# Kernel tuning notes

Hardware: AMD Instinct MI355X
Metric: run time of the kernel (lower is better)

Reference implementation:

```python
import jax, jax.numpy as jnp
import numpy as np


def setup_inputs() -> dict:
    key = jax.random.key(0)
    ks = jax.random.split(key, 8)
    B, C, W, H = 4, 256, 64, 64
    dqk = C // 8
    s_in = 1.0 / np.sqrt(C)
    return {
        "x": jax.random.normal(ks[0], (B, C, W, H), dtype=jnp.float32),
        "Wq": jax.random.normal(ks[1], (dqk, C), dtype=jnp.float32) * s_in,
        "bq": jnp.zeros((dqk,), dtype=jnp.float32),
        "Wk": jax.random.normal(ks[2], (dqk, C), dtype=jnp.float32) * s_in,
        "bk": jnp.zeros((dqk,), dtype=jnp.float32),
        "Wv": jax.random.normal(ks[3], (C, C), dtype=jnp.float32) * s_in,
        "bv": jnp.zeros((C,), dtype=jnp.float32),
        "gamma": jnp.zeros((1,), dtype=jnp.float32),
    }


def reference(x, Wq, bq, Wk, bk, Wv, bv, gamma):
    B, C, W, H = x.shape
    N = W * H
    xf = x.reshape(B, C, N)  # flatten spatial: B x C x N
    # 1x1 convs == per-pixel linear projections over channels
    q = jnp.einsum("bcn,dc->bnd", xf, Wq) + bq            # B x N x dqk
    k = jnp.einsum("bcn,dc->bdn", xf, Wk) + bk[None, :, None]  # B x dqk x N
    v = jnp.einsum("bcn,dc->bdn", xf, Wv) + bv[None, :, None]  # B x C x N
    # unscaled attention, softmax over keys (last dim)
    attn = jax.nn.softmax(jnp.einsum("bnd,bdm->bnm", q, k), axis=-1)  # B x N x N
    # out[b,c,i] = sum_j v[b,c,j] * attn[b,i,j]  (bmm with attn^T)
    out = jnp.einsum("bcj,bij->bci", v, attn).reshape(B, C, W, H)
    return gamma[0] * out + x
```

## Files before the change

kernel.cpp:

```cpp
#include <hip/hip_runtime.h>

#define BB 4
#define CC 256
#define NN 4096

typedef __attribute__((ext_vector_type(8))) short bh8;
typedef __attribute__((ext_vector_type(4))) float f32x4;

#define WPK_OFF  0
#define BALL_OFF 163840
#define QBF_OFF  165888
#define KBF_OFF  (165888 + 1048576)
#define VBF_OFF  (165888 + 2097152)

typedef const __attribute__((address_space(1))) void* gas_t;
typedef __attribute__((address_space(3))) void* las_t;
__device__ inline void gld16(const void* g, void* l) {
    __builtin_amdgcn_global_load_lds((gas_t)g, (las_t)l, 16, 0, 0);
}

__device__ inline int pack2bf(float a, float b) {
    unsigned ua = __builtin_bit_cast(unsigned, a) + 0x8000u;
    unsigned ub = __builtin_bit_cast(unsigned, b) + 0x8000u;
    return (int)__builtin_amdgcn_perm(ub, ua, 0x07060302u);
}
__device__ inline short f2bf1(float a) {
    return (short)((__builtin_bit_cast(unsigned, a) + 0x8000u) >> 16);
}

__global__ __launch_bounds__(256) void prep_w(const float* __restrict__ Wq,
        const float* __restrict__ bq, const float* __restrict__ Wk,
        const float* __restrict__ bk, const float* __restrict__ Wv,
        const float* __restrict__ bv, short* __restrict__ Wpk,
        float* __restrict__ ball) {
    int tid = blockIdx.x * 256 + threadIdx.x;
    if (tid < 10240) {
        int lane = tid & 63;
        int fc = tid >> 6;
        int mt = fc >> 3, ck = fc & 7;
        int m = mt * 16 + (lane & 15);
        int c0 = ck * 32 + (lane >> 4) * 8;
        const float* wrow;
        if (m < 32)      wrow = Wq + m * 256;
        else if (m < 64) wrow = Wk + (m - 32) * 256;
        else             wrow = Wv + (m - 64) * 256;
        int d[4];
        #pragma unroll
        for (int p = 0; p < 4; ++p)
            d[p] = pack2bf(wrow[c0 + 2 * p], wrow[c0 + 2 * p + 1]);
        *(int4*)(Wpk + tid * 8) = make_int4(d[0], d[1], d[2], d[3]);
    }
    if (tid < 320) {
        float b2 = tid < 32 ? bq[tid] : (tid < 64 ? bk[tid - 32] : bv[tid - 64]);
        ball[tid] = b2;
    }
}

__global__ __launch_bounds__(256) void proj(const float* __restrict__ x,
        const short* __restrict__ Wpk, const float* __restrict__ ball,
        short* __restrict__ qbf, short* __restrict__ kbf,
        short* __restrict__ vbf) {
    int t = threadIdx.x;
    int w = t >> 6, lane = t & 63, quad = lane >> 4, c15 = lane & 15;
    int tile = blockIdx.x;
    int b = tile >> 8, n0 = (tile & 255) * 16;
    const float* xb = x + (size_t)b * CC * NN;

    bh8 af[8];
    #pragma unroll
    for (int ck = 0; ck < 8; ++ck) {
        float v[8];
        #pragma unroll
        for (int e = 0; e < 8; ++e)
            v[e] = xb[(size_t)(ck * 32 + quad * 8 + e) * NN + n0 + c15];
        int d[4];
        #pragma unroll
        for (int p = 0; p < 4; ++p) d[p] = pack2bf(v[2 * p], v[2 * p + 1]);
        af[ck] = __builtin_bit_cast(bh8, make_int4(d[0], d[1], d[2], d[3]));
    }

    #pragma unroll
    for (int mti = 0; mti < 5; ++mti) {
        int mt = w * 5 + mti;
        float bl = ball[mt * 16 + c15];
        f32x4 acc = {bl, bl, bl, bl};
        #pragma unroll
        for (int ck = 0; ck < 8; ++ck) {
            bh8 wf = *(const bh8*)(Wpk + ((mt * 8 + ck) * 64 + lane) * 8);
            acc = __builtin_amdgcn_mfma_f32_16x16x32_bf16(af[ck], wf, acc, 0, 0, 0);
        }
        if (mt < 4) {
            short* dst = (mt < 2) ? qbf : kbf;
            int m = (mt & 1) * 16 + c15;
            #pragma unroll
            for (int r = 0; r < 4; ++r)
                dst[(size_t)(b * NN + n0 + quad * 4 + r) * 32 + m] = f2bf1(acc[r]);
        } else {
            int c = mt * 16 + c15 - 64;
            int2 pk;
            pk.x = pack2bf(acc[0], acc[1]);
            pk.y = pack2bf(acc[2], acc[3]);
            *(int2*)(vbf + (size_t)b * CC * NN + (size_t)c * NN + n0 + quad * 4) = pk;
        }
    }
}

__global__ __launch_bounds__(512, 2) void flash_attn(
        const short* __restrict__ qbf, const short* __restrict__ kbf,
        const short* __restrict__ vbf, const float* __restrict__ x,
        const float* __restrict__ gamma, float* __restrict__ out) {
    __shared__ char lds[81920];

    int bid = blockIdx.x;
    int b = bid & 3, i0 = (bid >> 2) * 64;
    int t = threadIdx.x;
    int w = t >> 6, lane = t & 63, quad = lane >> 4, c15 = lane & 15;
    int mg = w & 3, nh = w >> 2, jsub = w & 3;

    const short* qb = qbf + (size_t)b * NN * 32;
    const short* kb = kbf + (size_t)b * NN * 32;
    const short* vb = vbf + (size_t)b * CC * NN;

    bh8 qf0 = *(const bh8*)(qb + (size_t)(i0 + nh * 32 + c15) * 32 + quad * 8);
    bh8 qf1 = *(const bh8*)(qb + (size_t)(i0 + nh * 32 + 16 + c15) * 32 + quad * 8);

    int vrow = w * 32 + (lane >> 3);
    int glog = (lane & 7) ^ ((lane >> 3) & 7);
    const short* vsg = vb + (size_t)vrow * NN + glog * 8;
    char* vdst = lds + w * 4096;

    const short* kptr = kb + (size_t)(jsub * 16 + c15) * 32 + quad * 8;

    char* Pt = lds + 65536;
    float* lred = (float*)lds;

    f32x4 acc[4][2];
    #pragma unroll
    for (int ms = 0; ms < 4; ++ms) {
        acc[ms][0] = (f32x4){0.f, 0.f, 0.f, 0.f};
        acc[ms][1] = (f32x4){0.f, 0.f, 0.f, 0.f};
    }
    float lsum0 = 0.f, lsum1 = 0.f;
    const f32x4 initc = {-12.f, -12.f, -12.f, -12.f};

    #pragma unroll
    for (int r = 0; r < 4; ++r) gld16(vsg + r * 8 * NN, vdst + r * 1024);
    bh8 kf = *(const bh8*)kptr;
    __syncthreads();

    for (int jt = 0; jt < 64; ++jt) {
        int cur = jt & 1;
        f32x4 sa0 = __builtin_amdgcn_mfma_f32_16x16x32_bf16(kf, qf0, initc, 0, 0, 0);
        f32x4 sa1 = __builtin_amdgcn_mfma_f32_16x16x32_bf16(kf, qf1, initc, 0, 0, 0);
        bh8 kfn = *(const bh8*)(kptr + (size_t)((jt + 1) & 63) * 2048);
        float p0[4], p1[4];
        #pragma unroll
        for (int r = 0; r < 4; ++r) {
            p0[r] = __expf(sa0[r]); lsum0 += p0[r];
            p1[r] = __expf(sa1[r]); lsum1 += p1[r];
        }
        char* Ptc = Pt + cur * 8192;
        int g = jsub * 2 + (quad >> 1);
        int pb0 = (nh * 32 + c15) * 128 + ((g ^ (c15 & 7)) * 16) + (quad & 1) * 8;
        *(int2*)(Ptc + pb0) = make_int2(pack2bf(p0[0], p0[1]), pack2bf(p0[2], p0[3]));
        *(int2*)(Ptc + pb0 + 2048) = make_int2(pack2bf(p1[0], p1[1]), pack2bf(p1[2], p1[3]));

        __syncthreads();

        if (jt < 63) {
            const short* vs = vsg + (jt + 1) * 64;
            char* vd = vdst + ((cur ^ 1) << 15);
            #pragma unroll
            for (int r = 0; r < 4; ++r) gld16(vs + r * 8 * NN, vd + r * 1024);
        }

        const char* Vb = lds + cur * 32768;
        #pragma unroll
        for (int kk = 0; kk < 2; ++kk) {
            int gs = ((kk * 4 + quad) ^ (c15 & 7)) * 16;
            bh8 pfa = *(const bh8*)(Ptc + (nh * 32 + c15) * 128 + gs);
            bh8 pfb = *(const bh8*)(Ptc + (nh * 32 + 16 + c15) * 128 + gs);
            #pragma unroll
            for (int ms = 0; ms < 4; ++ms) {
                int c = mg * 64 + ms * 16 + c15;
                bh8 vf = *(const bh8*)(Vb + c * 128 + gs);
                acc[ms][0] = __builtin_amdgcn_mfma_f32_16x16x32_bf16(vf, pfa, acc[ms][0], 0, 0, 0);
                acc[ms][1] = __builtin_amdgcn_mfma_f32_16x16x32_bf16(vf, pfb, acc[ms][1], 0, 0, 0);
            }
        }
        kf = kfn;
    }

    lsum0 += __shfl_xor(lsum0, 16); lsum0 += __shfl_xor(lsum0, 32);
    lsum1 += __shfl_xor(lsum1, 16); lsum1 += __shfl_xor(lsum1, 32);
    __syncthreads();
    if (lane < 16) {
        lred[w * 32 + lane] = lsum0;
        lred[w * 32 + 16 + lane] = lsum1;
    }
    __syncthreads();
    float l0 = lred[(nh * 4 + 0) * 32 + c15] + lred[(nh * 4 + 1) * 32 + c15]
             + lred[(nh * 4 + 2) * 32 + c15] + lred[(nh * 4 + 3) * 32 + c15];
    float l1 = lred[(nh * 4 + 0) * 32 + 16 + c15] + lred[(nh * 4 + 1) * 32 + 16 + c15]
             + lred[(nh * 4 + 2) * 32 + 16 + c15] + lred[(nh * 4 + 3) * 32 + 16 + c15];
    float linv0 = 1.0f / l0, linv1 = 1.0f / l1;

    float gm = gamma[0];
    const float* xb2 = x + (size_t)b * CC * NN;
    float* ob = out + (size_t)b * CC * NN;
    int ia = i0 + nh * 32 + c15, ib2 = ia + 16;
    #pragma unroll
    for (int ms = 0; ms < 4; ++ms) {
        #pragma unroll
        for (int r = 0; r < 4; ++r) {
            int c = mg * 64 + ms * 16 + quad * 4 + r;
            ob[(size_t)c * NN + ia]  = gm * acc[ms][0][r] * linv0 + xb2[(size_t)c * NN + ia];
            ob[(size_t)c * NN + ib2] = gm * acc[ms][1][r] * linv1 + xb2[(size_t)c * NN + ib2];
        }
    }
}

extern "C" void kernel_launch(void* const* d_in, const int* in_sizes, int n_in,
                              void* d_out, int out_size, void* d_ws, size_t ws_size,
                              hipStream_t stream) {
    const float* x     = (const float*)d_in[0];
    const float* Wq    = (const float*)d_in[1];
    const float* bq    = (const float*)d_in[2];
    const float* Wk    = (const float*)d_in[3];
    const float* bk    = (const float*)d_in[4];
    const float* Wv    = (const float*)d_in[5];
    const float* bv    = (const float*)d_in[6];
    const float* gamma = (const float*)d_in[7];
    float* out = (float*)d_out;
    char*  ws  = (char*)d_ws;
    short* Wpk  = (short*)(ws + WPK_OFF);
    float* ball = (float*)(ws + BALL_OFF);
    short* qbf  = (short*)(ws + QBF_OFF);
    short* kbf  = (short*)(ws + KBF_OFF);
    short* vbf  = (short*)(ws + VBF_OFF);

    prep_w<<<40, 256, 0, stream>>>(Wq, bq, Wk, bk, Wv, bv, Wpk, ball);
    proj<<<1024, 256, 0, stream>>>(x, Wpk, ball, qbf, kbf, vbf);
    flash_attn<<<256, 512, 0, stream>>>(qbf, kbf, vbf, x, gamma, out);
}
```

Baseline: 146.3 us.

## Load V fragments directly from global into registers, drop V LDS staging

```diff
diff --git a/kernel.cpp b/kernel.cpp
--- a/kernel.cpp
+++ b/kernel.cpp
@@ -109,13 +109,13 @@
         const short* __restrict__ qbf, const short* __restrict__ kbf,
         const short* __restrict__ vbf, const float* __restrict__ x,
         const float* __restrict__ gamma, float* __restrict__ out) {
-    __shared__ char lds[81920];
+    __shared__ char lds[17408];
 
     int bid = blockIdx.x;
     int b = bid & 3, i0 = (bid >> 2) * 64;
     int t = threadIdx.x;
     int w = t >> 6, lane = t & 63, quad = lane >> 4, c15 = lane & 15;
-    int mg = w & 3, nh = w >> 2, jsub = w & 3;
+    int nh = w >> 2, jsub = w & 3;
 
     const short* qb = qbf + (size_t)b * NN * 32;
     const short* kb = kbf + (size_t)b * NN * 32;
@@ -124,35 +124,36 @@
     bh8 qf0 = *(const bh8*)(qb + (size_t)(i0 + nh * 32 + c15) * 32 + quad * 8);
     bh8 qf1 = *(const bh8*)(qb + (size_t)(i0 + nh * 32 + 16 + c15) * 32 + quad * 8);
 
-    int vrow = w * 32 + (lane >> 3);
-    int glog = (lane & 7) ^ ((lane >> 3) & 7);
-    const short* vsg = vb + (size_t)vrow * NN + glog * 8;
-    char* vdst = lds + w * 4096;
-
     const short* kptr = kb + (size_t)(jsub * 16 + c15) * 32 + quad * 8;
 
-    char* Pt = lds + 65536;
-    float* lred = (float*)lds;
-
-    f32x4 acc[4][2];
-    #pragma unroll
-    for (int ms = 0; ms < 4; ++ms) {
-        acc[ms][0] = (f32x4){0.f, 0.f, 0.f, 0.f};
-        acc[ms][1] = (f32x4){0.f, 0.f, 0.f, 0.f};
-    }
+    const short* vp0 = vb + (size_t)(w * 32 + c15) * NN + quad * 8;
+    const short* vp1 = vp0 + (size_t)16 * NN;
+
+    char* Pt = lds;
+    float* lred = (float*)(lds + 16384);
+
+    f32x4 acc[2][4];
+    #pragma unroll
+    for (int ms = 0; ms < 2; ++ms)
+        #pragma unroll
+        for (int f = 0; f < 4; ++f) acc[ms][f] = (f32x4){0.f, 0.f, 0.f, 0.f};
+
     float lsum0 = 0.f, lsum1 = 0.f;
     const f32x4 initc = {-12.f, -12.f, -12.f, -12.f};
 
-    #pragma unroll
-    for (int r = 0; r < 4; ++r) gld16(vsg + r * 8 * NN, vdst + r * 1024);
     bh8 kf = *(const bh8*)kptr;
-    __syncthreads();
 
     for (int jt = 0; jt < 64; ++jt) {
         int cur = jt & 1;
+        bh8 kfn = *(const bh8*)(kptr + (size_t)((jt + 1) & 63) * 2048);
+        size_t jo = (size_t)jt * 64;
+        bh8 vf00 = *(const bh8*)(vp0 + jo);
+        bh8 vf01 = *(const bh8*)(vp1 + jo);
+        bh8 vf10 = *(const bh8*)(vp0 + jo + 32);
+        bh8 vf11 = *(const bh8*)(vp1 + jo + 32);
+
         f32x4 sa0 = __builtin_amdgcn_mfma_f32_16x16x32_bf16(kf, qf0, initc, 0, 0, 0);
         f32x4 sa1 = __builtin_amdgcn_mfma_f32_16x16x32_bf16(kf, qf1, initc, 0, 0, 0);
-        bh8 kfn = *(const bh8*)(kptr + (size_t)((jt + 1) & 63) * 2048);
         float p0[4], p1[4];
         #pragma unroll
         for (int r = 0; r < 4; ++r) {
@@ -167,55 +168,54 @@
 
         __syncthreads();
 
-        if (jt < 63) {
-            const short* vs = vsg + (jt + 1) * 64;
-            char* vd = vdst + ((cur ^ 1) << 15);
-            #pragma unroll
-            for (int r = 0; r < 4; ++r) gld16(vs + r * 8 * NN, vd + r * 1024);
-        }
-
-        const char* Vb = lds + cur * 32768;
         #pragma unroll
         for (int kk = 0; kk < 2; ++kk) {
             int gs = ((kk * 4 + quad) ^ (c15 & 7)) * 16;
-            bh8 pfa = *(const bh8*)(Ptc + (nh * 32 + c15) * 128 + gs);
-            bh8 pfb = *(const bh8*)(Ptc + (nh * 32 + 16 + c15) * 128 + gs);
-            #pragma unroll
-            for (int ms = 0; ms < 4; ++ms) {
-                int c = mg * 64 + ms * 16 + c15;
-                bh8 vf = *(const bh8*)(Vb + c * 128 + gs);
-                acc[ms][0] = __builtin_amdgcn_mfma_f32_16x16x32_bf16(vf, pfa, acc[ms][0], 0, 0, 0);
-                acc[ms][1] = __builtin_amdgcn_mfma_f32_16x16x32_bf16(vf, pfb, acc[ms][1], 0, 0, 0);
-            }
+            bh8 pf[4];
+            #pragma unroll
+            for (int f = 0; f < 4; ++f)
+                pf[f] = *(const bh8*)(Ptc + (f * 16 + c15) * 128 + gs);
+            bh8 va = kk ? vf10 : vf00;
+            bh8 vbb = kk ? vf11 : vf01;
+            #pragma unroll
+            for (int f = 0; f < 4; ++f)
+                acc[0][f] = __builtin_amdgcn_mfma_f32_16x16x32_bf16(va, pf[f], acc[0][f], 0, 0, 0);
+            #pragma unroll
+            for (int f = 0; f < 4; ++f)
+                acc[1][f] = __builtin_amdgcn_mfma_f32_16x16x32_bf16(vbb, pf[f], acc[1][f], 0, 0, 0);
         }
         kf = kfn;
     }
 
     lsum0 += __shfl_xor(lsum0, 16); lsum0 += __shfl_xor(lsum0, 32);
     lsum1 += __shfl_xor(lsum1, 16); lsum1 += __shfl_xor(lsum1, 32);
-    __syncthreads();
     if (lane < 16) {
         lred[w * 32 + lane] = lsum0;
         lred[w * 32 + 16 + lane] = lsum1;
     }
     __syncthreads();
-    float l0 = lred[(nh * 4 + 0) * 32 + c15] + lred[(nh * 4 + 1) * 32 + c15]
-             + lred[(nh * 4 + 2) * 32 + c15] + lred[(nh * 4 + 3) * 32 + c15];
-    float l1 = lred[(nh * 4 + 0) * 32 + 16 + c15] + lred[(nh * 4 + 1) * 32 + 16 + c15]
-             + lred[(nh * 4 + 2) * 32 + 16 + c15] + lred[(nh * 4 + 3) * 32 + 16 + c15];
-    float linv0 = 1.0f / l0, linv1 = 1.0f / l1;
+    float linv[4];
+    #pragma unroll
+    for (int f = 0; f < 4; ++f) {
+        int base = (f >> 1) * 4 * 32 + (f & 1) * 16 + c15;
+        linv[f] = 1.0f / (lred[base] + lred[base + 32]
+                        + lred[base + 64] + lred[base + 96]);
+    }
 
     float gm = gamma[0];
     const float* xb2 = x + (size_t)b * CC * NN;
     float* ob = out + (size_t)b * CC * NN;
-    int ia = i0 + nh * 32 + c15, ib2 = ia + 16;
-    #pragma unroll
-    for (int ms = 0; ms < 4; ++ms) {
-        #pragma unroll
-        for (int r = 0; r < 4; ++r) {
-            int c = mg * 64 + ms * 16 + quad * 4 + r;
-            ob[(size_t)c * NN + ia]  = gm * acc[ms][0][r] * linv0 + xb2[(size_t)c * NN + ia];
-            ob[(size_t)c * NN + ib2] = gm * acc[ms][1][r] * linv1 + xb2[(size_t)c * NN + ib2];
+    #pragma unroll
+    for (int ms = 0; ms < 2; ++ms) {
+        #pragma unroll
+        for (int f = 0; f < 4; ++f) {
+            int i = i0 + f * 16 + c15;
+            #pragma unroll
+            for (int r = 0; r < 4; ++r) {
+                int c = w * 32 + ms * 16 + quad * 4 + r;
+                ob[(size_t)c * NN + i] = gm * acc[ms][f][r] * linv[f]
+                                       + xb2[(size_t)c * NN + i];
+            }
         }
     }
 }
```

Result: slower. 163.6 us (+11.8%).

## Process two key tiles per barrier with four-deep V and P LDS buffering

Applied to the files above, without the earlier changes.

```diff
diff --git a/kernel.cpp b/kernel.cpp
--- a/kernel.cpp
+++ b/kernel.cpp
@@ -109,7 +109,7 @@
         const short* __restrict__ qbf, const short* __restrict__ kbf,
         const short* __restrict__ vbf, const float* __restrict__ x,
         const float* __restrict__ gamma, float* __restrict__ out) {
-    __shared__ char lds[81920];
+    __shared__ char lds[163840];
 
     int bid = blockIdx.x;
     int b = bid & 3, i0 = (bid >> 2) * 64;
@@ -127,11 +127,10 @@
     int vrow = w * 32 + (lane >> 3);
     int glog = (lane & 7) ^ ((lane >> 3) & 7);
     const short* vsg = vb + (size_t)vrow * NN + glog * 8;
-    char* vdst = lds + w * 4096;
 
     const short* kptr = kb + (size_t)(jsub * 16 + c15) * 32 + quad * 8;
 
-    char* Pt = lds + 65536;
+    char* Pt = lds + 131072;
     float* lred = (float*)lds;
 
     f32x4 acc[4][2];
@@ -144,51 +143,73 @@
     const f32x4 initc = {-12.f, -12.f, -12.f, -12.f};
 
     #pragma unroll
-    for (int r = 0; r < 4; ++r) gld16(vsg + r * 8 * NN, vdst + r * 1024);
-    bh8 kf = *(const bh8*)kptr;
+    for (int r = 0; r < 4; ++r) gld16(vsg + r * 8 * NN, lds + w * 4096 + r * 1024);
+    #pragma unroll
+    for (int r = 0; r < 4; ++r) gld16(vsg + 64 + r * 8 * NN, lds + 32768 + w * 4096 + r * 1024);
+    bh8 kfa = *(const bh8*)kptr;
+    bh8 kfb = *(const bh8*)(kptr + 2048);
     __syncthreads();
 
-    for (int jt = 0; jt < 64; ++jt) {
-        int cur = jt & 1;
-        f32x4 sa0 = __builtin_amdgcn_mfma_f32_16x16x32_bf16(kf, qf0, initc, 0, 0, 0);
-        f32x4 sa1 = __builtin_amdgcn_mfma_f32_16x16x32_bf16(kf, qf1, initc, 0, 0, 0);
-        bh8 kfn = *(const bh8*)(kptr + (size_t)((jt + 1) & 63) * 2048);
-        float p0[4], p1[4];
+    int g = jsub * 2 + (quad >> 1);
+    int pb0 = (nh * 32 + c15) * 128 + ((g ^ (c15 & 7)) * 16) + (quad & 1) * 8;
+
+    for (int pr = 0; pr < 32; ++pr) {
+        int jt0 = pr * 2, jt1 = jt0 + 1;
+        int ba = jt0 & 3, bb = jt1 & 3;
+        f32x4 sa0a = __builtin_amdgcn_mfma_f32_16x16x32_bf16(kfa, qf0, initc, 0, 0, 0);
+        f32x4 sa1a = __builtin_amdgcn_mfma_f32_16x16x32_bf16(kfa, qf1, initc, 0, 0, 0);
+        f32x4 sa0b = __builtin_amdgcn_mfma_f32_16x16x32_bf16(kfb, qf0, initc, 0, 0, 0);
+        f32x4 sa1b = __builtin_amdgcn_mfma_f32_16x16x32_bf16(kfb, qf1, initc, 0, 0, 0);
+        bh8 kfan = *(const bh8*)(kptr + (size_t)((jt0 + 2) & 63) * 2048);
+        bh8 kfbn = *(const bh8*)(kptr + (size_t)((jt1 + 2) & 63) * 2048);
+        float pa0[4], pa1[4], pb0v[4], pb1v[4];
         #pragma unroll
         for (int r = 0; r < 4; ++r) {
-            p0[r] = __expf(sa0[r]); lsum0 += p0[r];
-            p1[r] = __expf(sa1[r]); lsum1 += p1[r];
-        }
-        char* Ptc = Pt + cur * 8192;
-        int g = jsub * 2 + (quad >> 1);
-        int pb0 = (nh * 32 + c15) * 128 + ((g ^ (c15 & 7)) * 16) + (quad & 1) * 8;
-        *(int2*)(Ptc + pb0) = make_int2(pack2bf(p0[0], p0[1]), pack2bf(p0[2], p0[3]));
-        *(int2*)(Ptc + pb0 + 2048) = make_int2(pack2bf(p1[0], p1[1]), pack2bf(p1[2], p1[3]));
+            pa0[r] = __expf(sa0a[r]); lsum0 += pa0[r];
+            pa1[r] = __expf(sa1a[r]); lsum1 += pa1[r];
+            pb0v[r] = __expf(sa0b[r]); lsum0 += pb0v[r];
+            pb1v[r] = __expf(sa1b[r]); lsum1 += pb1v[r];
+        }
+        char* Pa = Pt + ba * 8192;
+        char* Pb = Pt + bb * 8192;
+        *(int2*)(Pa + pb0) = make_int2(pack2bf(pa0[0], pa0[1]), pack2bf(pa0[2], pa0[3]));
+        *(int2*)(Pa + pb0 + 2048) = make_int2(pack2bf(pa1[0], pa1[1]), pack2bf(pa1[2], pa1[3]));
+        *(int2*)(Pb + pb0) = make_int2(pack2bf(pb0v[0], pb0v[1]), pack2bf(pb0v[2], pb0v[3]));
+        *(int2*)(Pb + pb0 + 2048) = make_int2(pack2bf(pb1v[0], pb1v[1]), pack2bf(pb1v[2], pb1v[3]));
 
         __syncthreads();
 
-        if (jt < 63) {
-            const short* vs = vsg + (jt + 1) * 64;
-            char* vd = vdst + ((cur ^ 1) << 15);
-            #pragma unroll
-            for (int r = 0; r < 4; ++r) gld16(vs + r * 8 * NN, vd + r * 1024);
-        }
-
-        const char* Vb = lds + cur * 32768;
-        #pragma unroll
-        for (int kk = 0; kk < 2; ++kk) {
-            int gs = ((kk * 4 + quad) ^ (c15 & 7)) * 16;
-            bh8 pfa = *(const bh8*)(Ptc + (nh * 32 + c15) * 128 + gs);
-            bh8 pfb = *(const bh8*)(Ptc + (nh * 32 + 16 + c15) * 128 + gs);
-            #pragma unroll
-            for (int ms = 0; ms < 4; ++ms) {
-                int c = mg * 64 + ms * 16 + c15;
-                bh8 vf = *(const bh8*)(Vb + c * 128 + gs);
-                acc[ms][0] = __builtin_amdgcn_mfma_f32_16x16x32_bf16(vf, pfa, acc[ms][0], 0, 0, 0);
-                acc[ms][1] = __builtin_amdgcn_mfma_f32_16x16x32_bf16(vf, pfb, acc[ms][1], 0, 0, 0);
+        {
+            const short* vsA = vsg + (size_t)((jt0 + 2) & 63) * 64;
+            const short* vsB = vsg + (size_t)((jt1 + 2) & 63) * 64;
+            char* vdA = lds + (size_t)(ba ^ 2) * 32768 + w * 4096;
+            char* vdB = lds + (size_t)(bb ^ 2) * 32768 + w * 4096;
+            #pragma unroll
+            for (int r = 0; r < 4; ++r) gld16(vsA + r * 8 * NN, vdA + r * 1024);
+            #pragma unroll
+            for (int r = 0; r < 4; ++r) gld16(vsB + r * 8 * NN, vdB + r * 1024);
+        }
+
+        #pragma unroll
+        for (int st = 0; st < 2; ++st) {
+            const char* Vb = lds + (size_t)(st ? bb : ba) * 32768;
+            const char* Ptc = st ? Pb : Pa;
+            #pragma unroll
+            for (int kk = 0; kk < 2; ++kk) {
+                int gs = ((kk * 4 + quad) ^ (c15 & 7)) * 16;
+                bh8 pfa = *(const bh8*)(Ptc + (nh * 32 + c15) * 128 + gs);
+                bh8 pfb = *(const bh8*)(Ptc + (nh * 32 + 16 + c15) * 128 + gs);
+                #pragma unroll
+                for (int ms = 0; ms < 4; ++ms) {
+                    int c = mg * 64 + ms * 16 + c15;
+                    bh8 vf = *(const bh8*)(Vb + c * 128 + gs);
+                    acc[ms][0] = __builtin_amdgcn_mfma_f32_16x16x32_bf16(vf, pfa, acc[ms][0], 0, 0, 0);
+                    acc[ms][1] = __builtin_amdgcn_mfma_f32_16x16x32_bf16(vf, pfb, acc[ms][1], 0, 0, 0);
+                }
             }
         }
-        kf = kfn;
+        kfa = kfan;
+        kfb = kfbn;
     }
 
     lsum0 += __shfl_xor(lsum0, 16); lsum0 += __shfl_xor(lsum0, 32);
```

After: 144.6 us. Within noise of the previous version (-1.2%).

## Keep P in registers and split keys across waves with LDS reduction

Applied to the files above, without the earlier changes.

```diff
diff --git a/kernel.cpp b/kernel.cpp
--- a/kernel.cpp
+++ b/kernel.cpp
@@ -5,6 +5,7 @@
 #define NN 4096
 
 typedef __attribute__((ext_vector_type(8))) short bh8;
+typedef __attribute__((ext_vector_type(4))) short bh4;
 typedef __attribute__((ext_vector_type(4))) float f32x4;
 
 #define WPK_OFF  0
@@ -109,36 +110,35 @@
         const short* __restrict__ qbf, const short* __restrict__ kbf,
         const short* __restrict__ vbf, const float* __restrict__ x,
         const float* __restrict__ gamma, float* __restrict__ out) {
-    __shared__ char lds[81920];
+    __shared__ char lds[136192];
 
     int bid = blockIdx.x;
     int b = bid & 3, i0 = (bid >> 2) * 64;
     int t = threadIdx.x;
     int w = t >> 6, lane = t & 63, quad = lane >> 4, c15 = lane & 15;
-    int mg = w & 3, nh = w >> 2, jsub = w & 3;
+    int jsub = w & 3, ih = w >> 2;
 
     const short* qb = qbf + (size_t)b * NN * 32;
     const short* kb = kbf + (size_t)b * NN * 32;
     const short* vb = vbf + (size_t)b * CC * NN;
 
-    bh8 qf0 = *(const bh8*)(qb + (size_t)(i0 + nh * 32 + c15) * 32 + quad * 8);
-    bh8 qf1 = *(const bh8*)(qb + (size_t)(i0 + nh * 32 + 16 + c15) * 32 + quad * 8);
-
-    int vrow = w * 32 + (lane >> 3);
+    bh8 qf0 = *(const bh8*)(qb + (size_t)(i0 + ih * 32 + c15) * 32 + quad * 8);
+    bh8 qf1 = *(const bh8*)(qb + (size_t)(i0 + ih * 32 + 16 + c15) * 32 + quad * 8);
+
     int glog = (lane & 7) ^ ((lane >> 3) & 7);
-    const short* vsg = vb + (size_t)vrow * NN + glog * 8;
+    const short* vsg = vb + (size_t)(w * 32 + (lane >> 3)) * NN + glog * 8;
     char* vdst = lds + w * 4096;
 
     const short* kptr = kb + (size_t)(jsub * 16 + c15) * 32 + quad * 8;
 
-    char* Pt = lds + 65536;
-    float* lred = (float*)lds;
-
-    f32x4 acc[4][2];
-    #pragma unroll
-    for (int ms = 0; ms < 4; ++ms) {
-        acc[ms][0] = (f32x4){0.f, 0.f, 0.f, 0.f};
-        acc[ms][1] = (f32x4){0.f, 0.f, 0.f, 0.f};
+    int gb = jsub * 2 + (quad >> 1);
+    int vrd = c15 * 128 + ((gb ^ (c15 & 7)) << 4) + (quad & 1) * 8;
+
+    f32x4 acc[16][2];
+    #pragma unroll
+    for (int cb = 0; cb < 16; ++cb) {
+        acc[cb][0] = (f32x4){0.f, 0.f, 0.f, 0.f};
+        acc[cb][1] = (f32x4){0.f, 0.f, 0.f, 0.f};
     }
     float lsum0 = 0.f, lsum1 = 0.f;
     const f32x4 initc = {-12.f, -12.f, -12.f, -12.f};
@@ -159,11 +159,10 @@
             p0[r] = __expf(sa0[r]); lsum0 += p0[r];
             p1[r] = __expf(sa1[r]); lsum1 += p1[r];
         }
-        char* Ptc = Pt + cur * 8192;
-        int g = jsub * 2 + (quad >> 1);
-        int pb0 = (nh * 32 + c15) * 128 + ((g ^ (c15 & 7)) * 16) + (quad & 1) * 8;
-        *(int2*)(Ptc + pb0) = make_int2(pack2bf(p0[0], p0[1]), pack2bf(p0[2], p0[3]));
-        *(int2*)(Ptc + pb0 + 2048) = make_int2(pack2bf(p1[0], p1[1]), pack2bf(p1[2], p1[3]));
+        int2 a2 = make_int2(pack2bf(p0[0], p0[1]), pack2bf(p0[2], p0[3]));
+        int2 b2 = make_int2(pack2bf(p1[0], p1[1]), pack2bf(p1[2], p1[3]));
+        bh4 pA = __builtin_bit_cast(bh4, a2);
+        bh4 pB = __builtin_bit_cast(bh4, b2);
 
         __syncthreads();
 
@@ -176,47 +175,66 @@
 
         const char* Vb = lds + cur * 32768;
         #pragma unroll
-        for (int kk = 0; kk < 2; ++kk) {
-            int gs = ((kk * 4 + quad) ^ (c15 & 7)) * 16;
-            bh8 pfa = *(const bh8*)(Ptc + (nh * 32 + c15) * 128 + gs);
-            bh8 pfb = *(const bh8*)(Ptc + (nh * 32 + 16 + c15) * 128 + gs);
-            #pragma unroll
-            for (int ms = 0; ms < 4; ++ms) {
-                int c = mg * 64 + ms * 16 + c15;
-                bh8 vf = *(const bh8*)(Vb + c * 128 + gs);
-                acc[ms][0] = __builtin_amdgcn_mfma_f32_16x16x32_bf16(vf, pfa, acc[ms][0], 0, 0, 0);
-                acc[ms][1] = __builtin_amdgcn_mfma_f32_16x16x32_bf16(vf, pfb, acc[ms][1], 0, 0, 0);
-            }
+        for (int cb = 0; cb < 16; ++cb) {
+            bh4 vf = *(const bh4*)(Vb + cb * 2048 + vrd);
+            acc[cb][0] = __builtin_amdgcn_mfma_f32_16x16x16bf16_1k(vf, pA, acc[cb][0], 0, 0, 0);
+            acc[cb][1] = __builtin_amdgcn_mfma_f32_16x16x16bf16_1k(vf, pB, acc[cb][1], 0, 0, 0);
         }
         kf = kfn;
     }
 
     lsum0 += __shfl_xor(lsum0, 16); lsum0 += __shfl_xor(lsum0, 32);
     lsum1 += __shfl_xor(lsum1, 16); lsum1 += __shfl_xor(lsum1, 32);
-    __syncthreads();
+
+    float* ored = (float*)lds;
+    float* lred = (float*)(lds + 135168);
+
+    __syncthreads();
+
     if (lane < 16) {
         lred[w * 32 + lane] = lsum0;
         lred[w * 32 + 16 + lane] = lsum1;
     }
-    __syncthreads();
-    float l0 = lred[(nh * 4 + 0) * 32 + c15] + lred[(nh * 4 + 1) * 32 + c15]
-             + lred[(nh * 4 + 2) * 32 + c15] + lred[(nh * 4 + 3) * 32 + c15];
-    float l1 = lred[(nh * 4 + 0) * 32 + 16 + c15] + lred[(nh * 4 + 1) * 32 + 16 + c15]
-             + lred[(nh * 4 + 2) * 32 + 16 + c15] + lred[(nh * 4 + 3) * 32 + 16 + c15];
-    float linv0 = 1.0f / l0, linv1 = 1.0f / l1;
-
+    if (jsub >= 2) {
+        float* rg = ored + (size_t)(ih * 2 + (jsub - 2)) * 8448;
+        #pragma unroll
+        for (int cb = 0; cb < 16; ++cb)
+            #pragma unroll
+            for (int f = 0; f < 2; ++f)
+                #pragma unroll
+                for (int r = 0; r < 4; ++r)
+                    rg[(cb * 16 + quad * 4 + r) * 33 + f * 16 + c15] = acc[cb][f][r];
+    }
+    __syncthreads();
+    if (jsub < 2) {
+        float* rg = ored + (size_t)(ih * 2 + jsub) * 8448;
+        #pragma unroll
+        for (int cb = 0; cb < 16; ++cb)
+            #pragma unroll
+            for (int f = 0; f < 2; ++f)
+                #pragma unroll
+                for (int r = 0; r < 4; ++r) {
+                    int idx = (cb * 16 + quad * 4 + r) * 33 + f * 16 + c15;
+                    rg[idx] += acc[cb][f][r];
+                }
+    }
+    __syncthreads();
+    int il = lane & 31, ch = lane >> 5;
+    float lv = 0.f;
+    #pragma unroll
+    for (int js = 0; js < 4; ++js) lv += lred[(ih * 4 + js) * 32 + il];
+    float linv = 1.0f / lv;
     float gm = gamma[0];
     const float* xb2 = x + (size_t)b * CC * NN;
     float* ob = out + (size_t)b * CC * NN;
-    int ia = i0 + nh * 32 + c15, ib2 = ia + 16;
-    #pragma unroll
-    for (int ms = 0; ms < 4; ++ms) {
-        #pragma unroll
-        for (int r = 0; r < 4; ++r) {
-            int c = mg * 64 + ms * 16 + quad * 4 + r;
-            ob[(size_t)c * NN + ia]  = gm * acc[ms][0][r] * linv0 + xb2[(size_t)c * NN + ia];
-            ob[(size_t)c * NN + ib2] = gm * acc[ms][1][r] * linv1 + xb2[(size_t)c * NN + ib2];
-        }
+    int i = i0 + ih * 32 + il;
+    const float* rgA = ored + (size_t)(ih * 2 + 0) * 8448;
+    const float* rgB = ored + (size_t)(ih * 2 + 1) * 8448;
+    #pragma unroll 4
+    for (int rr = 0; rr < 32; ++rr) {
+        int c = jsub * 64 + rr * 2 + ch;
+        float v = rgA[c * 33 + il] + rgB[c * 33 + il];
+        ob[(size_t)c * NN + i] = gm * v * linv + xb2[(size_t)c * NN + i];
     }
 }
 
```

Result: slower. 153.1 us (+4.6%).
